# Optimization experiments

Hardware: AMD Instinct MI355X
Metric: run time of the kernel (lower is better)

## Reference

```python
import jax, jax.numpy as jnp
import numpy as np

EMB = 32
STEPS = 3
SLOPE = 0.01  # LeakyReLU default negative slope


def lrelu(x):
    return jnp.where(x > 0, x, SLOPE * x)


def seg_softmax(logits, seg, num_seg):
    # numerically stable per-segment softmax (matches torch_geometric.utils.softmax)
    m = jax.ops.segment_max(logits, seg, num_segments=num_seg)
    e = jnp.exp(logits - m[seg])
    s = jax.ops.segment_sum(e, seg, num_segments=num_seg)
    return e / s[seg]


def setup_inputs() -> dict:
    key = jax.random.key(0)
    ks = jax.random.split(key, 32)
    N, E, G = 200000, 3200000, 128
    p = lambda k, shape: (jax.random.normal(k, shape, dtype=jnp.float32) * 0.1)
    inp = {
        "node_feats": jax.random.normal(ks[0], (N, 1), dtype=jnp.float32),
        "edge_index": jax.random.randint(ks[1], (2, E), 0, N),
        "batch": jnp.sort(jax.random.randint(ks[2], (N,), 0, G)),
        "num_graphs": G,
        # embed_node: Linear(1, 32)
        "W_embed": p(ks[3], (1, EMB)), "b_embed": p(ks[4], (EMB,)),
        # per-step GraphNet params (stacked over steps)
        "Wm": p(ks[5], (STEPS, EMB, EMB)), "bm": p(ks[6], (STEPS, EMB)),          # f_mess (edge_size=0)
        "Wa": p(ks[7], (STEPS, 3 * EMB, EMB)), "ba": p(ks[8], (STEPS, EMB)),      # f_agg: [x, xg, agg]
        # per-step GlobalNode params
        "Wgate": p(ks[9], (STEPS, EMB, 1)), "bgate": p(ks[10], (STEPS, 1)),       # att_mask
        "Wfeat": p(ks[11], (STEPS, EMB, EMB)), "bfeat": p(ks[12], (STEPS, EMB)),  # att_feat
        "Wt": p(ks[13], (STEPS, 2 * EMB, EMB)), "bt": p(ks[14], (STEPS, EMB)),    # transform
        # heads
        "W_v": p(ks[15], (EMB, 1)), "b_v": p(ks[16], (1,)),
        "W_a0": p(ks[17], (EMB, 2)), "b_a0": p(ks[18], (2,)),
        "W_a1": p(ks[19], (EMB, 1)), "b_a1": p(ks[20], (1,)),
    }
    return inp


def reference(node_feats, edge_index, batch, num_graphs,
              W_embed, b_embed, Wm, bm, Wa, ba, Wgate, bgate, Wfeat, bfeat,
              Wt, bt, W_v, b_v, W_a0, b_a0, W_a1, b_a1):
    N = node_feats.shape[0]
    src, dst = edge_index[0], edge_index[1]

    x = lrelu(node_feats @ W_embed + b_embed)            # [N, 32]
    xg = jnp.zeros((num_graphs, EMB), dtype=x.dtype)     # [G, 32]

    for i in range(Wm.shape[0]):
        # GraphNet: gather -> MLP -> scatter-max -> update MLP + residual
        msg = lrelu(x[src] @ Wm[i] + bm[i])              # [E, 32]
        agg = jax.ops.segment_max(msg, dst, num_segments=N)
        agg = jnp.where(jnp.isfinite(agg), agg, 0.0)     # empty segments -> 0
        z = jnp.concatenate([x, xg[batch], agg], axis=1)  # [N, 96]
        x = lrelu(z @ Wa[i] + ba[i]) + x

        # GlobalNode: GlobalAttention pooling + transform with residual
        gate = seg_softmax((x @ Wgate[i] + bgate[i])[:, 0], batch, num_graphs)  # [N]
        feat = lrelu(x @ Wfeat[i] + bfeat[i])            # [N, 32]
        pooled = jax.ops.segment_sum(gate[:, None] * feat, batch, num_segments=num_graphs)
        cat = jnp.concatenate([pooled, xg], axis=1)      # [G, 64]
        xg = lrelu(cat @ Wt[i] + bt[i]) + xg

    value = xg @ W_v + b_v                               # [G, 1]
    a0_probs = jax.nn.softmax(xg @ W_a0 + b_a0, axis=1)  # [G, 2]
    a1_softmax = seg_softmax((x @ W_a1 + b_a1)[:, 0], batch, num_graphs)  # [N]
    return value, a0_probs, a1_softmax
```

## Files before the change

kernel.cpp:

```cpp
#include <hip/hip_runtime.h>
#include <hip/hip_bf16.h>

#define GG 128
#define SLOPE 0.01f
#define CHUNK 8192
#define NPB 64
#define NREP 64

#define OFF_Wm   0
#define OFF_bm   3072
#define OFF_Wa   3168
#define OFF_ba   12384
#define OFF_Wg   12480
#define OFF_bg   12576
#define OFF_Wf   12592
#define OFF_bf   15664
#define OFF_Wt   15760
#define OFF_bt   21904
#define OFF_Wa1  22000
#define OFF_ba1  22032
#define WCAT_N   22048

__device__ __forceinline__ float lrelu(float v) { return v > 0.f ? v : SLOPE * v; }

__device__ __forceinline__ float ldf(const void* p, int i, int isf) {
    if (isf) return ((const float*)p)[i];
    return __bfloat162float(((const __hip_bfloat16*)p)[i]);
}
__device__ __forceinline__ void stf(void* p, int i, float v, int isf) {
    if (isf) ((float*)p)[i] = v;
    else ((__hip_bfloat16*)p)[i] = __float2bfloat16(v);
}

__device__ __forceinline__ float bfLo(unsigned u) { return __uint_as_float(u << 16); }
__device__ __forceinline__ float bfHi(unsigned u) { return __uint_as_float(u & 0xFFFF0000u); }

__global__ void k_detect(const unsigned short* __restrict__ w, int n, int* __restrict__ flag,
                         unsigned* __restrict__ bcnt, int B) {
    __shared__ int bad;
    for (int t = threadIdx.x; t <= B; t += 256) bcnt[t] = 0u;
    if (threadIdx.x == 0) bad = 0;
    __syncthreads();
    for (int t = threadIdx.x; t < n; t += 256) {
        unsigned short u = w[t];
        int e = (u >> 7) & 0xFF;
        if (e >= 141) bad = 1;
    }
    __syncthreads();
    if (threadIdx.x == 0) { flag[0] = bad; flag[32] = 1; }
}

struct CvtArgs {
    const void* p[12];
    int off[12];
    int n[12];
};
__global__ void k_prep(CvtArgs a, float* __restrict__ wcat, const int* __restrict__ dtf,
                       const void* __restrict__ ba0, float* __restrict__ xgw,
                       const int* __restrict__ batch, int* __restrict__ goff, int N,
                       const int* __restrict__ dst, unsigned* __restrict__ bcnt, int E, int B,
                       float* __restrict__ xg_a, float* __restrict__ U, float* __restrict__ S) {
    __shared__ unsigned h[2048];
    int blk = blockIdx.x;
    int tid = threadIdx.x;
    const int cG = (N + 255) >> 8;
    const int cH = (E + CHUNK - 1) / CHUNK;
    if (blk < 432) {
        int seg = blk / 36;
        int i = (blk % 36) * 256 + tid;
        int isf = *dtf;
        if (i < a.n[seg]) wcat[a.off[seg] + i] = ldf(a.p[seg], i, isf);
        return;
    }
    blk -= 432;
    if (blk < 16) {
        int isf = *dtf;
        int idx = blk * 256 + tid;
        xgw[idx] = ldf(ba0, idx & 31, isf);
        return;
    }
    blk -= 16;
    if (blk < cG) {
        int n = blk * 256 + tid;
        if (n >= N) return;
        int bn = batch[n];
        if (n == 0) {
            for (int g = 0; g <= bn; ++g) goff[g] = 0;
        } else {
            int bp = batch[n - 1];
            for (int g = bp + 1; g <= bn; ++g) goff[g] = n;
        }
        if (n == N - 1) {
            for (int g = bn + 1; g <= GG; ++g) goff[g] = N;
        }
        return;
    }
    blk -= cG;
    if (blk < cH) {
        if (B > 2048) return;
        for (int t = tid; t < B; t += 256) h[t] = 0;
        __syncthreads();
        int start = blk * CHUNK, end = min(E, start + CHUNK);
        for (int e = start + tid; e < end; e += 256)
            atomicAdd(&h[dst[e] >> 8], 1u);
        __syncthreads();
        for (int t = tid; t < B; t += 256)
            if (h[t]) atomicAdd(&bcnt[t], h[t]);
        return;
    }
    blk -= cH;
    {
        float4 z4 = make_float4(0.f, 0.f, 0.f, 0.f);
        long long fi = (long long)blk * 256 + tid;
        if (fi < 65536) { ((float4*)U)[fi] = z4; return; }
        fi -= 65536;
        if (fi < 2048) { ((float4*)S)[fi] = z4; return; }
        fi -= 2048;
        if (fi < 1024) { ((float4*)xg_a)[fi] = z4; return; }
    }
}

__global__ void k_hist(const int* __restrict__ dst, unsigned* __restrict__ deg, int E) {
    int e = blockIdx.x * 256 + threadIdx.x;
    if (e >= E) return;
    atomicAdd(&deg[dst[e]], 1u);
}
__global__ void k_scan1(const unsigned* __restrict__ deg, unsigned* __restrict__ excl,
                        unsigned* __restrict__ bsum, int N) {
    __shared__ unsigned s[256];
    int i = blockIdx.x * 256 + threadIdx.x;
    unsigned v = (i < N) ? deg[i] : 0u;
    s[threadIdx.x] = v;
    __syncthreads();
    for (int off = 1; off < 256; off <<= 1) {
        unsigned t = (threadIdx.x >= (unsigned)off) ? s[threadIdx.x - off] : 0u;
        __syncthreads();
        s[threadIdx.x] += t;
        __syncthreads();
    }
    if (i < N) excl[i] = s[threadIdx.x] - v;
    if (threadIdx.x == 255) bsum[blockIdx.x] = s[255];
}
__global__ void k_scan2(const unsigned* __restrict__ bsum, unsigned* __restrict__ boff, int nb) {
    __shared__ unsigned s[256];
    __shared__ unsigned carry;
    if (threadIdx.x == 0) carry = 0u;
    __syncthreads();
    for (int base = 0; base < nb; base += 256) {
        int i = base + threadIdx.x;
        unsigned v = (i < nb) ? bsum[i] : 0u;
        s[threadIdx.x] = v;
        __syncthreads();
        for (int off = 1; off < 256; off <<= 1) {
            unsigned t = (threadIdx.x >= (unsigned)off) ? s[threadIdx.x - off] : 0u;
            __syncthreads();
            s[threadIdx.x] += t;
            __syncthreads();
        }
        if (i < nb) boff[i] = carry + s[threadIdx.x] - v;
        __syncthreads();
        if (threadIdx.x == 0) carry += s[255];
        __syncthreads();
    }
}
__global__ void k_scan3(unsigned* __restrict__ indptr, const unsigned* __restrict__ boff,
                        unsigned* __restrict__ cursor, int N, int E) {
    int i = blockIdx.x * 256 + threadIdx.x;
    if (i >= N) return;
    unsigned v = indptr[i] + boff[i >> 8];
    indptr[i] = v;
    cursor[i] = v;
    if (i == 0) indptr[N] = (unsigned)E;
}
__global__ void k_scatter(const int* __restrict__ src, const int* __restrict__ dst,
                          unsigned* __restrict__ cursor, unsigned* __restrict__ ssrc, int E) {
    int e = blockIdx.x * 256 + threadIdx.x;
    if (e >= E) return;
    unsigned pos = atomicAdd(&cursor[dst[e]], 1u);
    ssrc[pos] = (unsigned)src[e];
}

__global__ void k_bscan(const unsigned* __restrict__ bcnt, unsigned* __restrict__ bbase,
                        unsigned* __restrict__ bcur, int B, int E) {
    __shared__ unsigned s[256];
    __shared__ unsigned carry;
    if (threadIdx.x == 0) carry = 0u;
    __syncthreads();
    for (int base = 0; base < B; base += 256) {
        int i = base + threadIdx.x;
        unsigned v = (i < B) ? bcnt[i] : 0u;
        s[threadIdx.x] = v;
        __syncthreads();
        for (int off = 1; off < 256; off <<= 1) {
            unsigned t = (threadIdx.x >= (unsigned)off) ? s[threadIdx.x - off] : 0u;
            __syncthreads();
            s[threadIdx.x] += t;
            __syncthreads();
        }
        if (i < B) {
            unsigned ex = carry + s[threadIdx.x] - v;
            bbase[i] = ex;
            bcur[i] = ex;
        }
        __syncthreads();
        if (threadIdx.x == 0) carry += s[255];
        __syncthreads();
    }
    if (threadIdx.x == 0) bbase[B] = (unsigned)E;
}

__global__ void k_work(const int* __restrict__ src, const int* __restrict__ dst,
                       unsigned* __restrict__ bcur, unsigned long long* __restrict__ packed,
                       int E, int B, int nbA,
                       const void* __restrict__ nf, const void* __restrict__ We,
                       const void* __restrict__ be,
                       const float* __restrict__ Wm0, const float* __restrict__ bm0,
                       float* __restrict__ x, __hip_bfloat16* __restrict__ m, int N,
                       const int* __restrict__ dtf) {
    __shared__ unsigned h[2048];
    __shared__ unsigned pos[2048];
    __shared__ float WL[1024];
    __shared__ float WeL[32], beL[32], bmL[32];
    __shared__ float xs[8][32];
    int tid = threadIdx.x;
    if ((int)blockIdx.x < nbA) {
        for (int t = tid; t < B; t += 256) h[t] = 0;
        __syncthreads();
        int start = blockIdx.x * CHUNK, end = min(E, start + CHUNK);
        for (int e = start + tid; e < end; e += 256)
            atomicAdd(&h[dst[e] >> 8], 1u);
        __syncthreads();
        for (int t = tid; t < B; t += 256)
            pos[t] = h[t] ? atomicAdd(&bcur[t], h[t]) : 0u;
        __syncthreads();
        for (int e = start + tid; e < end; e += 256) {
            int d = dst[e];
            unsigned p = atomicAdd(&pos[d >> 8], 1u);
            packed[p] = ((unsigned long long)(unsigned)d << 32) | (unsigned)src[e];
        }
        return;
    }
    int blkE = blockIdx.x - nbA;
    int isf = *dtf;
    for (int t = tid; t < 1024; t += 256) WL[t] = Wm0[t];
    if (tid < 32) { WeL[tid] = ldf(We, tid, isf); beL[tid] = ldf(be, tid, isf); bmL[tid] = bm0[tid]; }
    int s = tid >> 5, j = tid & 31;
    int n = blkE * 8 + s;
    __syncthreads();
    float xv = 0.f;
    if (n < N) {
        xv = lrelu(ldf(nf, n, isf) * WeL[j] + beL[j]);
        x[n * 32 + j] = xv;
        xs[s][j] = xv;
    }
    __syncthreads();
    if (n >= N) return;
    float acc = bmL[j];
#pragma unroll
    for (int k = 0; k < 32; ++k) acc += xs[s][k] * WL[k * 32 + j];
    m[n * 32 + j] = __float2bfloat16(lrelu(acc));
}

__global__ void k_csr(const unsigned long long* __restrict__ packed,
                      const unsigned* __restrict__ bbase,
                      unsigned* __restrict__ indptr,
                      unsigned* __restrict__ ssrc, int N, int E) {
    __shared__ unsigned deg[256];
    __shared__ unsigned scn[256];
    __shared__ unsigned cur[256];
    int g = blockIdx.x, tid = threadIdx.x;
    int n0 = g << 8;
    int cnt = min(256, N - n0);
    deg[tid] = 0;
    __syncthreads();
    unsigned e0 = bbase[g], e1 = bbase[g + 1];
    for (unsigned e = e0 + tid; e < e1; e += 256) {
        int d = (int)(packed[e] >> 32);
        atomicAdd(&deg[d - n0], 1u);
    }
    __syncthreads();
    unsigned v = deg[tid];
    scn[tid] = v;
    __syncthreads();
    for (int off = 1; off < 256; off <<= 1) {
        unsigned t = (tid >= off) ? scn[tid - off] : 0u;
        __syncthreads();
        scn[tid] += t;
        __syncthreads();
    }
    unsigned start = e0 + scn[tid] - v;
    if (tid < cnt) { indptr[n0 + tid] = start; cur[tid] = start; }
    if (g == (int)gridDim.x - 1 && tid == 0) indptr[N] = (unsigned)E;
    __syncthreads();
    for (unsigned e = e0 + tid; e < e1; e += 256) {
        unsigned long long pk = packed[e];
        int d = (int)(pk >> 32);
        unsigned p = atomicAdd(&cur[d - n0], 1u);
        ssrc[p] = (unsigned)pk;
    }
}

__global__ __launch_bounds__(256, 4)
void k_step(float* __restrict__ x, const __hip_bfloat16* __restrict__ m_in,
            __hip_bfloat16* __restrict__ m_out,
            const int* __restrict__ batch,
            const unsigned* __restrict__ indptr, const unsigned* __restrict__ ssrc,
            const float* __restrict__ Wa, const float* __restrict__ xgw,
            const float* __restrict__ Wg, const float* __restrict__ bg,
            const float* __restrict__ Wa1, const float* __restrict__ ba1,
            const float* __restrict__ Wf, const float* __restrict__ bf,
            const float* __restrict__ Wm_nx, const float* __restrict__ bm_nx,
            float* __restrict__ la1, float* __restrict__ U, float* __restrict__ S,
            int N, int hasNext) {
    __shared__ float WL[2048];
    __shared__ float WmL[1024];
    __shared__ float zL[8][64];
    __shared__ float xnL[8][32];
    __shared__ float WgL[32], W1L[32], bmL[32], bfL[32];
    __shared__ float bgL, b1L;
    int tid = threadIdx.x;
    for (int t = tid; t < 2048; t += 256) WL[t] = (t < 1024) ? Wa[t] : Wa[t + 1024];
    if (hasNext) {
        for (int t = tid; t < 1024; t += 256) WmL[t] = Wm_nx[t];
        if (tid < 32) bmL[tid] = bm_nx[tid];
    }
    if (tid < 32) { WgL[tid] = Wg[tid]; W1L[tid] = Wa1[tid]; bfL[tid] = bf[tid]; }
    if (tid == 0) { bgL = bg[0]; b1L = ba1[0]; }
    int s = tid >> 5, j = tid & 31;
    int c = j & 7, eo = j >> 3;
    float wfr[32];
#pragma unroll
    for (int k = 0; k < 32; ++k) wfr[k] = Wf[k * 32 + j];
    const uint2* m2 = (const uint2*)m_in;
    int nbase = blockIdx.x * NPB;
    int rep = blockIdx.x & (NREP - 1);
    float* Urep = U + (size_t)rep * GG * 32;
    float* Srep = S + (size_t)rep * GG;
    __syncthreads();
    int gcur = -1;
    float Uacc = 0.f, Sacc = 0.f;
    for (int sub = 0; sub < NPB / 8; ++sub) {
        int n = nbase + sub * 8 + s;
        bool valid = n < N;
        int gb = gcur;
        float xj = 0.f;
        if (valid) {
            xj = x[n * 32 + j];
            zL[s][j] = xj;
            gb = batch[n];
        }
        if (valid && gb != gcur) {
            if (gcur >= 0) {
                atomicAdd(&Urep[gcur * 32 + j], Uacc);
                if (j == 0) atomicAdd(&Srep[gcur], Sacc);
            }
            gcur = gb; Uacc = 0.f; Sacc = 0.f;
        }
        unsigned st = 0, en = 0;
        if (valid) { st = indptr[n]; en = indptr[n + 1]; }
        float a[4];
#pragma unroll
        for (int t = 0; t < 4; ++t) a[t] = -INFINITY;
        if (en > st) {
            unsigned last = en - 1;
            for (unsigned base = st; base < en; base += 32) {
                unsigned eA = min(base + eo, last);
                unsigned eB = min(base + 4 + eo, last);
                unsigned eC = min(base + 8 + eo, last);
                unsigned eD = min(base + 12 + eo, last);
                unsigned eE = min(base + 16 + eo, last);
                unsigned eF = min(base + 20 + eo, last);
                unsigned eG = min(base + 24 + eo, last);
                unsigned eH = min(base + 28 + eo, last);
                unsigned sA = ssrc[eA];
                unsigned sB = ssrc[eB];
                unsigned sC = ssrc[eC];
                unsigned sD = ssrc[eD];
                unsigned sE = ssrc[eE];
                unsigned sF = ssrc[eF];
                unsigned sG = ssrc[eG];
                unsigned sH = ssrc[eH];
                uint2 vA = m2[sA * 8 + c];
                uint2 vB = m2[sB * 8 + c];
                uint2 vC = m2[sC * 8 + c];
                uint2 vD = m2[sD * 8 + c];
                uint2 vE = m2[sE * 8 + c];
                uint2 vF = m2[sF * 8 + c];
                uint2 vG = m2[sG * 8 + c];
                uint2 vH = m2[sH * 8 + c];
                a[0] = fmaxf(a[0], fmaxf(fmaxf(fmaxf(bfLo(vA.x), bfLo(vB.x)), fmaxf(bfLo(vC.x), bfLo(vD.x))),
                                         fmaxf(fmaxf(bfLo(vE.x), bfLo(vF.x)), fmaxf(bfLo(vG.x), bfLo(vH.x)))));
                a[1] = fmaxf(a[1], fmaxf(fmaxf(fmaxf(bfHi(vA.x), bfHi(vB.x)), fmaxf(bfHi(vC.x), bfHi(vD.x))),
                                         fmaxf(fmaxf(bfHi(vE.x), bfHi(vF.x)), fmaxf(bfHi(vG.x), bfHi(vH.x)))));
                a[2] = fmaxf(a[2], fmaxf(fmaxf(fmaxf(bfLo(vA.y), bfLo(vB.y)), fmaxf(bfLo(vC.y), bfLo(vD.y))),
                                         fmaxf(fmaxf(bfLo(vE.y), bfLo(vF.y)), fmaxf(bfLo(vG.y), bfLo(vH.y)))));
                a[3] = fmaxf(a[3], fmaxf(fmaxf(fmaxf(bfHi(vA.y), bfHi(vB.y)), fmaxf(bfHi(vC.y), bfHi(vD.y))),
                                         fmaxf(fmaxf(bfHi(vE.y), bfHi(vF.y)), fmaxf(bfHi(vG.y), bfHi(vH.y)))));
            }
        }
#pragma unroll
        for (int t = 0; t < 4; ++t) {
            a[t] = fmaxf(a[t], __shfl_xor(a[t], 8));
            a[t] = fmaxf(a[t], __shfl_xor(a[t], 16));
        }
        if (valid && eo == 0) {
            bool empty = (st == en);
#pragma unroll
            for (int t = 0; t < 4; ++t)
                zL[s][32 + (c << 2) + t] = empty ? 0.f : a[t];
        }
        if (valid) {
            float acc0 = xgw[gb * 32 + j];
            float acc1 = 0.f;
#pragma unroll
            for (int k = 0; k < 64; k += 2) {
                acc0 += zL[s][k] * WL[k * 32 + j];
                acc1 += zL[s][k + 1] * WL[(k + 1) * 32 + j];
            }
            float xn = lrelu(acc0 + acc1) + xj;
            x[n * 32 + j] = xn;
            xnL[s][j] = xn;
            float lv = xn * WgL[j];
            if (hasNext) {
#pragma unroll
                for (int off = 16; off; off >>= 1) lv += __shfl_xor(lv, off);
            } else {
                float l1 = xn * W1L[j];
#pragma unroll
                for (int off = 16; off; off >>= 1) { lv += __shfl_xor(lv, off); l1 += __shfl_xor(l1, off); }
                if (j == 0) la1[n] = l1 + b1L;
            }
            float e = __expf(lv + bgL);
            float f = bfL[j];
            if (hasNext) {
                float a2 = bmL[j];
#pragma unroll
                for (int k = 0; k < 32; ++k) {
                    float v = xnL[s][k];
                    f += v * wfr[k];
                    a2 += v * WmL[k * 32 + j];
                }
                m_out[n * 32 + j] = __float2bfloat16(lrelu(a2));
            } else {
#pragma unroll
                for (int k = 0; k < 32; ++k) f += xnL[s][k] * wfr[k];
            }
            Uacc += e * lrelu(f);
            Sacc += e;
        }
    }
    if (gcur >= 0) {
        atomicAdd(&Urep[gcur * 32 + j], Uacc);
        if (j == 0) atomicAdd(&Srep[gcur], Sacc);
    }
}

__global__ void k_gupd(float* __restrict__ U, float* __restrict__ S,
                       const float* __restrict__ xg_in,
                       const float* __restrict__ Wt, const float* __restrict__ bt,
                       float* __restrict__ xg_out,
                       const float* __restrict__ WaNx, const float* __restrict__ baNx,
                       float* __restrict__ xgw, int hasNext,
                       const float* __restrict__ logits, const int* __restrict__ goff,
                       const void* __restrict__ Wv, const void* __restrict__ bv,
                       const void* __restrict__ Wa0, const void* __restrict__ ba0,
                       void* __restrict__ out, int N, const int* __restrict__ dtf) {
    __shared__ float Up[8][32];
    __shared__ float Sp[8];
    __shared__ float pl[32];
    __shared__ float vL[32];
    __shared__ float red[256];
    int g = blockIdx.x;
    int tid = threadIdx.x;
    int rp = tid >> 5, j = tid & 31;
    float usum = 0.f, ssum = 0.f;
    for (int r = rp; r < NREP; r += 8) {
        size_t ui = (size_t)r * GG * 32 + g * 32 + j;
        usum += U[ui];
        U[ui] = 0.f;
        if (j == 0) { ssum += S[r * GG + g]; S[r * GG + g] = 0.f; }
    }
    Up[rp][j] = usum;
    if (j == 0) Sp[rp] = ssum;
    __syncthreads();
    if (rp == 0) {
        float ut = 0.f;
#pragma unroll
        for (int i = 0; i < 8; ++i) ut += Up[i][j];
        float st = ((Sp[0] + Sp[1]) + (Sp[2] + Sp[3])) + ((Sp[4] + Sp[5]) + (Sp[6] + Sp[7]));
        float inv = (st > 0.f) ? 1.f / st : 0.f;
        pl[j] = ut * inv;
        float xgv = xg_in[g * 32 + j];
        vL[j] = xgv;
        float acc = bt[j];
#pragma unroll
        for (int k = 0; k < 32; ++k) acc += pl[k] * Wt[k * 32 + j];
#pragma unroll
        for (int k = 0; k < 32; ++k) acc += vL[k] * Wt[(32 + k) * 32 + j];
        float v = lrelu(acc) + xgv;
        xg_out[g * 32 + j] = v;
        vL[j] = v;
        if (hasNext) {
            float aw = baNx[j];
#pragma unroll
            for (int k = 0; k < 32; ++k) aw += vL[k] * WaNx[(32 + k) * 32 + j];
            xgw[g * 32 + j] = aw;
        }
    }
    __syncthreads();
    if (hasNext) return;
    int isf = *dtf;
    int s0 = goff[g], s1 = goff[g + 1];
    float lm = -INFINITY;
    for (int n = s0 + tid; n < s1; n += 256) lm = fmaxf(lm, logits[n]);
    red[tid] = lm;
    __syncthreads();
    for (int off = 128; off; off >>= 1) {
        if (tid < off) red[tid] = fmaxf(red[tid], red[tid + off]);
        __syncthreads();
    }
    float gmax = red[0];
    __syncthreads();
    float ls = 0.f;
    for (int n = s0 + tid; n < s1; n += 256) ls += expf(logits[n] - gmax);
    red[tid] = ls;
    __syncthreads();
    for (int off = 128; off; off >>= 1) {
        if (tid < off) red[tid] += red[tid + off];
        __syncthreads();
    }
    float inv = (red[0] > 0.f) ? 1.f / red[0] : 0.f;
    __syncthreads();
    for (int n = s0 + tid; n < s1; n += 256)
        stf(out, 384 + n, expf(logits[n] - gmax) * inv, isf);
    if (tid == 0) {
        float acc = ldf(bv, 0, isf);
        for (int k = 0; k < 32; ++k) acc += vL[k] * ldf(Wv, k, isf);
        stf(out, g, acc, isf);
        float l0 = ldf(ba0, 0, isf), l1 = ldf(ba0, 1, isf);
        for (int k = 0; k < 32; ++k) {
            float xv = vL[k];
            l0 += xv * ldf(Wa0, k * 2, isf);
            l1 += xv * ldf(Wa0, k * 2 + 1, isf);
        }
        float mm = fmaxf(l0, l1);
        float e0 = expf(l0 - mm), e1 = expf(l1 - mm);
        float si = 1.f / (e0 + e1);
        stf(out, 128 + 2 * g, e0 * si, isf);
        stf(out, 128 + 2 * g + 1, e1 * si, isf);
    }
}

extern "C" void kernel_launch(void* const* d_in, const int* in_sizes, int n_in,
                              void* d_out, int out_size, void* d_ws, size_t ws_size,
                              hipStream_t stream) {
    const void* nf      = d_in[0];
    const int*  eidx    = (const int*)d_in[1];
    const int*  batch   = (const int*)d_in[2];
    const void* W_embed = d_in[4];
    const void* b_embed = d_in[5];
    const void* Wm      = d_in[6];
    const void* bm      = d_in[7];
    const void* Wa      = d_in[8];
    const void* ba      = d_in[9];
    const void* Wgate   = d_in[10];
    const void* bgate   = d_in[11];
    const void* Wfeat   = d_in[12];
    const void* bfeat   = d_in[13];
    const void* Wt      = d_in[14];
    const void* bt      = d_in[15];
    const void* W_v     = d_in[16];
    const void* b_v     = d_in[17];
    const void* W_a0    = d_in[18];
    const void* b_a0    = d_in[19];
    const void* W_a1    = d_in[20];
    const void* b_a1    = d_in[21];

    const int N = in_sizes[0];
    const int E = in_sizes[1] / 2;
    const int nWm = in_sizes[6];
    const int* src = eidx;
    const int* dst = eidx + E;
    const int B = (N + 255) >> 8;

    char* ws = (char*)d_ws;
    size_t off = 0;
    auto alloc = [&](size_t bytes) -> char* {
        char* p = ws + off;
        off = (off + bytes + 255) & ~(size_t)255;
        return p;
    };
    float*          x      = (float*)alloc((size_t)N * 32 * 4);
    size_t mBytes  = (size_t)N * 32 * 2;
    __hip_bfloat16*     m_a    = (__hip_bfloat16*)alloc(mBytes);
    __hip_bfloat16*     m_b    = (__hip_bfloat16*)alloc(mBytes);
    unsigned long long* packed = (unsigned long long*)alloc((size_t)E * 8);
    float*          la1    = (float*)alloc((size_t)N * 4);
    unsigned*       indptr = (unsigned*)alloc((size_t)(N + 1) * 4);
    unsigned*       cursor = (unsigned*)alloc((size_t)N * 4);
    unsigned*       ssrc   = (unsigned*)alloc((size_t)(E + 16) * 4);
    const int nb = (N + 255) / 256;
    unsigned*       bsum   = (unsigned*)alloc((size_t)nb * 4);
    unsigned*       boff   = (unsigned*)alloc((size_t)nb * 4);
    unsigned*       bcnt   = (unsigned*)alloc((size_t)(B + 1) * 4);
    unsigned*       bbase  = (unsigned*)alloc((size_t)(B + 1) * 4);
    unsigned*       bcur   = (unsigned*)alloc((size_t)(B + 1) * 4);
    int*            goff   = (int*)alloc((size_t)(GG + 1) * 4);
    float*          xg_a   = (float*)alloc((size_t)GG * 32 * 4);
    float*          xg_b   = (float*)alloc((size_t)GG * 32 * 4);
    float*          xgw    = (float*)alloc((size_t)GG * 32 * 4);
    float*          U      = (float*)alloc((size_t)NREP * GG * 32 * 4);
    float*          S      = (float*)alloc((size_t)NREP * GG * 4);
    int*            dtf    = (int*)alloc(256);
    float*          wcat   = (float*)alloc((size_t)WCAT_N * 4);

    const int nB_n  = (N + 255) / 256;
    const int nB_e  = (E + 255) / 256;
    const int nB_n8 = (N + 7) / 8;
    const int nB_st = (N + NPB - 1) / NPB;
    const int nB_ch = (E + CHUNK - 1) / CHUNK;

    k_detect<<<1, 256, 0, stream>>>((const unsigned short*)Wm, nWm, dtf, bcnt, B);

    CvtArgs ca;
    const void* ps[12] = {Wm, bm, Wa, ba, Wgate, bgate, Wfeat, bfeat, Wt, bt, W_a1, b_a1};
    const int  offs[12] = {OFF_Wm, OFF_bm, OFF_Wa, OFF_ba, OFF_Wg, OFF_bg,
                           OFF_Wf, OFF_bf, OFF_Wt, OFF_bt, OFF_Wa1, OFF_ba1};
    const int  ns[12]  = {3072, 96, 9216, 96, 96, 3, 3072, 96, 6144, 96, 32, 1};
    for (int i = 0; i < 12; ++i) { ca.p[i] = ps[i]; ca.off[i] = offs[i]; ca.n[i] = ns[i]; }

    const int nPrep = 432 + 16 + nB_n + nB_ch + 268;
    k_prep<<<nPrep, 256, 0, stream>>>(ca, wcat, dtf, ba, xgw, batch, goff, N,
                                      dst, bcnt, E, B, xg_a, U, S);

    if (B <= 2048) {
        k_bscan<<<1, 256, 0, stream>>>(bcnt, bbase, bcur, B, E);
        k_work<<<nB_ch + nB_n8, 256, 0, stream>>>(src, dst, bcur, packed, E, B, nB_ch,
                                                  nf, W_embed, b_embed,
                                                  wcat + OFF_Wm, wcat + OFF_bm,
                                                  x, m_a, N, dtf);
        k_csr<<<B, 256, 0, stream>>>(packed, bbase, indptr, ssrc, N, E);
    } else {
        hipMemsetAsync(cursor, 0, (size_t)N * 4, stream);
        k_hist<<<nB_e, 256, 0, stream>>>(dst, cursor, E);
        k_scan1<<<nb, 256, 0, stream>>>(cursor, indptr, bsum, N);
        k_scan2<<<1, 256, 0, stream>>>(bsum, boff, nb);
        k_scan3<<<nB_n, 256, 0, stream>>>(indptr, boff, cursor, N, E);
        k_scatter<<<nB_e, 256, 0, stream>>>(src, dst, cursor, ssrc, E);
        k_work<<<nB_n8, 256, 0, stream>>>(src, dst, bcur, packed, E, B, 0,
                                          nf, W_embed, b_embed,
                                          wcat + OFF_Wm, wcat + OFF_bm,
                                          x, m_a, N, dtf);
    }

    float* xg_cur = xg_a;
    float* xg_nxt = xg_b;
    __hip_bfloat16* m_cur = m_a;
    __hip_bfloat16* m_nxt = m_b;
    for (int i = 0; i < 3; ++i) {
        int hasNext = (i < 2) ? 1 : 0;
        k_step<<<nB_st, 256, 0, stream>>>(x, m_cur, m_nxt, batch, indptr, ssrc,
                                          wcat + OFF_Wa + i * 3072, xgw,
                                          wcat + OFF_Wg + i * 32, wcat + OFF_bg + i,
                                          wcat + OFF_Wa1, wcat + OFF_ba1,
                                          wcat + OFF_Wf + i * 1024, wcat + OFF_bf + i * 32,
                                          wcat + OFF_Wm + (i + 1) * 1024,
                                          wcat + OFF_bm + (i + 1) * 32,
                                          la1, U, S, N, hasNext);
        k_gupd<<<GG, 256, 0, stream>>>(U, S, xg_cur,
                                       wcat + OFF_Wt + i * 2048,
                                       wcat + OFF_bt + i * 32, xg_nxt,
                                       wcat + OFF_Wa + (i + 1) * 3072,
                                       wcat + OFF_ba + (i + 1) * 32,
                                       xgw, hasNext,
                                       la1, goff, W_v, b_v, W_a0, b_a0,
                                       d_out, N, dtf);
        float* tmp = xg_cur; xg_cur = xg_nxt; xg_nxt = tmp;
        __hip_bfloat16* tm = m_cur; m_cur = m_nxt; m_nxt = tm;
    }
}
```

Measured before the change: 568.9 us.

## Software-pipeline node metadata and first edge-index batch across sub-iterations

Restructures the per-node aggregation loop into a software pipeline. Node metadata (x, batch, indptr) is loaded two sub-steps ahead, and the first 32 source indices one sub-step ahead, so the dependent gather chain indptr→ssrc→message overlaps with compute on the current node. It raises register pressure with many extra live values and loads clamped dummy data for out-of-range nodes, which may reduce occupancy.

```diff
diff --git a/kernel.cpp b/kernel.cpp
--- a/kernel.cpp
+++ b/kernel.cpp
@@ -339,86 +339,124 @@
     __syncthreads();
     int gcur = -1;
     float Uacc = 0.f, Sacc = 0.f;
+
+    int nC; bool vC; int gbC; float xjC; unsigned stC, enC;
+    int nN; bool vN; int gbN; float xjN; unsigned stN, enN;
+    unsigned p0, p1, p2, p3, p4, p5, p6, p7;
+    unsigned q0, q1, q2, q3, q4, q5, q6, q7;
+
+    auto loadMeta = [&](int sub, int& nn, bool& vv, int& gg, float& xx,
+                        unsigned& st_, unsigned& en_) {
+        int n = nbase + sub * 8 + s;
+        vv = (n < N);
+        int cl = vv ? n : (N - 1);
+        nn = cl;
+        xx = x[cl * 32 + j];
+        gg = batch[cl];
+        st_ = indptr[cl];
+        en_ = indptr[cl + 1];
+    };
+    auto issueSS = [&](unsigned st_, unsigned en_,
+                       unsigned& a0, unsigned& a1, unsigned& a2, unsigned& a3,
+                       unsigned& a4, unsigned& a5, unsigned& a6, unsigned& a7) {
+        unsigned b = (en_ > st_) ? st_ : 0u;
+        unsigned last = (en_ > st_) ? (en_ - 1) : 0u;
+        a0 = ssrc[min(b + eo, last)];
+        a1 = ssrc[min(b + 4 + eo, last)];
+        a2 = ssrc[min(b + 8 + eo, last)];
+        a3 = ssrc[min(b + 12 + eo, last)];
+        a4 = ssrc[min(b + 16 + eo, last)];
+        a5 = ssrc[min(b + 20 + eo, last)];
+        a6 = ssrc[min(b + 24 + eo, last)];
+        a7 = ssrc[min(b + 28 + eo, last)];
+    };
+
+    loadMeta(0, nC, vC, gbC, xjC, stC, enC);
+    issueSS(stC, enC, p0, p1, p2, p3, p4, p5, p6, p7);
+    loadMeta(1, nN, vN, gbN, xjN, stN, enN);
+
     for (int sub = 0; sub < NPB / 8; ++sub) {
-        int n = nbase + sub * 8 + s;
-        bool valid = n < N;
-        int gb = gcur;
-        float xj = 0.f;
-        if (valid) {
-            xj = x[n * 32 + j];
-            zL[s][j] = xj;
-            gb = batch[n];
-        }
-        if (valid && gb != gcur) {
-            if (gcur >= 0) {
-                atomicAdd(&Urep[gcur * 32 + j], Uacc);
-                if (j == 0) atomicAdd(&Srep[gcur], Sacc);
+        uint2 vA = m2[p0 * 8 + c];
+        uint2 vB = m2[p1 * 8 + c];
+        uint2 vC2 = m2[p2 * 8 + c];
+        uint2 vD = m2[p3 * 8 + c];
+        uint2 vE = m2[p4 * 8 + c];
+        uint2 vF = m2[p5 * 8 + c];
+        uint2 vG = m2[p6 * 8 + c];
+        uint2 vH = m2[p7 * 8 + c];
+        issueSS(stN, enN, q0, q1, q2, q3, q4, q5, q6, q7);
+        int nN2; bool vN2; int gbN2; float xjN2; unsigned stN2, enN2;
+        loadMeta(sub + 2, nN2, vN2, gbN2, xjN2, stN2, enN2);
+        float a0 = fmaxf(fmaxf(fmaxf(bfLo(vA.x), bfLo(vB.x)), fmaxf(bfLo(vC2.x), bfLo(vD.x))),
+                         fmaxf(fmaxf(bfLo(vE.x), bfLo(vF.x)), fmaxf(bfLo(vG.x), bfLo(vH.x))));
+        float a1 = fmaxf(fmaxf(fmaxf(bfHi(vA.x), bfHi(vB.x)), fmaxf(bfHi(vC2.x), bfHi(vD.x))),
+                         fmaxf(fmaxf(bfHi(vE.x), bfHi(vF.x)), fmaxf(bfHi(vG.x), bfHi(vH.x))));
+        float a2 = fmaxf(fmaxf(fmaxf(bfLo(vA.y), bfLo(vB.y)), fmaxf(bfLo(vC2.y), bfLo(vD.y))),
+                         fmaxf(fmaxf(bfLo(vE.y), bfLo(vF.y)), fmaxf(bfLo(vG.y), bfLo(vH.y))));
+        float a3 = fmaxf(fmaxf(fmaxf(bfHi(vA.y), bfHi(vB.y)), fmaxf(bfHi(vC2.y), bfHi(vD.y))),
+                         fmaxf(fmaxf(bfHi(vE.y), bfHi(vF.y)), fmaxf(bfHi(vG.y), bfHi(vH.y))));
+        if (enC > stC + 32) {
+            unsigned last = enC - 1;
+            for (unsigned base = stC + 32; base < enC; base += 32) {
+                unsigned tA = ssrc[min(base + eo, last)];
+                unsigned tB = ssrc[min(base + 4 + eo, last)];
+                unsigned tC = ssrc[min(base + 8 + eo, last)];
+                unsigned tD = ssrc[min(base + 12 + eo, last)];
+                unsigned tE = ssrc[min(base + 16 + eo, last)];
+                unsigned tF = ssrc[min(base + 20 + eo, last)];
+                unsigned tG = ssrc[min(base + 24 + eo, last)];
+                unsigned tH = ssrc[min(base + 28 + eo, last)];
+                uint2 wA = m2[tA * 8 + c];
+                uint2 wB = m2[tB * 8 + c];
+                uint2 wC = m2[tC * 8 + c];
+                uint2 wD = m2[tD * 8 + c];
+                uint2 wE = m2[tE * 8 + c];
+                uint2 wF = m2[tF * 8 + c];
+                uint2 wG = m2[tG * 8 + c];
+                uint2 wH = m2[tH * 8 + c];
+                a0 = fmaxf(a0, fmaxf(fmaxf(fmaxf(bfLo(wA.x), bfLo(wB.x)), fmaxf(bfLo(wC.x), bfLo(wD.x))),
+                                     fmaxf(fmaxf(bfLo(wE.x), bfLo(wF.x)), fmaxf(bfLo(wG.x), bfLo(wH.x)))));
+                a1 = fmaxf(a1, fmaxf(fmaxf(fmaxf(bfHi(wA.x), bfHi(wB.x)), fmaxf(bfHi(wC.x), bfHi(wD.x))),
+                                     fmaxf(fmaxf(bfHi(wE.x), bfHi(wF.x)), fmaxf(bfHi(wG.x), bfHi(wH.x)))));
+                a2 = fmaxf(a2, fmaxf(fmaxf(fmaxf(bfLo(wA.y), bfLo(wB.y)), fmaxf(bfLo(wC.y), bfLo(wD.y))),
+                                     fmaxf(fmaxf(bfLo(wE.y), bfLo(wF.y)), fmaxf(bfLo(wG.y), bfLo(wH.y)))));
+                a3 = fmaxf(a3, fmaxf(fmaxf(fmaxf(bfHi(wA.y), bfHi(wB.y)), fmaxf(bfHi(wC.y), bfHi(wD.y))),
+                                     fmaxf(fmaxf(bfHi(wE.y), bfHi(wF.y)), fmaxf(bfHi(wG.y), bfHi(wH.y)))));
             }
-            gcur = gb; Uacc = 0.f; Sacc = 0.f;
-        }
-        unsigned st = 0, en = 0;
-        if (valid) { st = indptr[n]; en = indptr[n + 1]; }
-        float a[4];
-#pragma unroll
-        for (int t = 0; t < 4; ++t) a[t] = -INFINITY;
-        if (en > st) {
-            unsigned last = en - 1;
-            for (unsigned base = st; base < en; base += 32) {
-                unsigned eA = min(base + eo, last);
-                unsigned eB = min(base + 4 + eo, last);
-                unsigned eC = min(base + 8 + eo, last);
-                unsigned eD = min(base + 12 + eo, last);
-                unsigned eE = min(base + 16 + eo, last);
-                unsigned eF = min(base + 20 + eo, last);
-                unsigned eG = min(base + 24 + eo, last);
-                unsigned eH = min(base + 28 + eo, last);
-                unsigned sA = ssrc[eA];
-                unsigned sB = ssrc[eB];
-                unsigned sC = ssrc[eC];
-                unsigned sD = ssrc[eD];
-                unsigned sE = ssrc[eE];
-                unsigned sF = ssrc[eF];
-                unsigned sG = ssrc[eG];
-                unsigned sH = ssrc[eH];
-                uint2 vA = m2[sA * 8 + c];
-                uint2 vB = m2[sB * 8 + c];
-                uint2 vC = m2[sC * 8 + c];
-                uint2 vD = m2[sD * 8 + c];
-                uint2 vE = m2[sE * 8 + c];
-                uint2 vF = m2[sF * 8 + c];
-                uint2 vG = m2[sG * 8 + c];
-                uint2 vH = m2[sH * 8 + c];
-                a[0] = fmaxf(a[0], fmaxf(fmaxf(fmaxf(bfLo(vA.x), bfLo(vB.x)), fmaxf(bfLo(vC.x), bfLo(vD.x))),
-                                         fmaxf(fmaxf(bfLo(vE.x), bfLo(vF.x)), fmaxf(bfLo(vG.x), bfLo(vH.x)))));
-                a[1] = fmaxf(a[1], fmaxf(fmaxf(fmaxf(bfHi(vA.x), bfHi(vB.x)), fmaxf(bfHi(vC.x), bfHi(vD.x))),
-                                         fmaxf(fmaxf(bfHi(vE.x), bfHi(vF.x)), fmaxf(bfHi(vG.x), bfHi(vH.x)))));
-                a[2] = fmaxf(a[2], fmaxf(fmaxf(fmaxf(bfLo(vA.y), bfLo(vB.y)), fmaxf(bfLo(vC.y), bfLo(vD.y))),
-                                         fmaxf(fmaxf(bfLo(vE.y), bfLo(vF.y)), fmaxf(bfLo(vG.y), bfLo(vH.y)))));
-                a[3] = fmaxf(a[3], fmaxf(fmaxf(fmaxf(bfHi(vA.y), bfHi(vB.y)), fmaxf(bfHi(vC.y), bfHi(vD.y))),
-                                         fmaxf(fmaxf(bfHi(vE.y), bfHi(vF.y)), fmaxf(bfHi(vG.y), bfHi(vH.y)))));
+        }
+        a0 = fmaxf(a0, __shfl_xor(a0, 8));
+        a0 = fmaxf(a0, __shfl_xor(a0, 16));
+        a1 = fmaxf(a1, __shfl_xor(a1, 8));
+        a1 = fmaxf(a1, __shfl_xor(a1, 16));
+        a2 = fmaxf(a2, __shfl_xor(a2, 8));
+        a2 = fmaxf(a2, __shfl_xor(a2, 16));
+        a3 = fmaxf(a3, __shfl_xor(a3, 8));
+        a3 = fmaxf(a3, __shfl_xor(a3, 16));
+        if (vC) {
+            if (gbC != gcur) {
+                if (gcur >= 0) {
+                    atomicAdd(&Urep[gcur * 32 + j], Uacc);
+                    if (j == 0) atomicAdd(&Srep[gcur], Sacc);
+                }
+                gcur = gbC; Uacc = 0.f; Sacc = 0.f;
             }
-        }
-#pragma unroll
-        for (int t = 0; t < 4; ++t) {
-            a[t] = fmaxf(a[t], __shfl_xor(a[t], 8));
-            a[t] = fmaxf(a[t], __shfl_xor(a[t], 16));
-        }
-        if (valid && eo == 0) {
-            bool empty = (st == en);
-#pragma unroll
-            for (int t = 0; t < 4; ++t)
-                zL[s][32 + (c << 2) + t] = empty ? 0.f : a[t];
-        }
-        if (valid) {
-            float acc0 = xgw[gb * 32 + j];
+            zL[s][j] = xjC;
+            if (eo == 0) {
+                bool empty = (stC == enC);
+                zL[s][32 + (c << 2) + 0] = empty ? 0.f : a0;
+                zL[s][32 + (c << 2) + 1] = empty ? 0.f : a1;
+                zL[s][32 + (c << 2) + 2] = empty ? 0.f : a2;
+                zL[s][32 + (c << 2) + 3] = empty ? 0.f : a3;
+            }
+            float acc0 = xgw[gbC * 32 + j];
             float acc1 = 0.f;
 #pragma unroll
             for (int k = 0; k < 64; k += 2) {
                 acc0 += zL[s][k] * WL[k * 32 + j];
                 acc1 += zL[s][k + 1] * WL[(k + 1) * 32 + j];
             }
-            float xn = lrelu(acc0 + acc1) + xj;
-            x[n * 32 + j] = xn;
+            float xn = lrelu(acc0 + acc1) + xjC;
+            x[nC * 32 + j] = xn;
             xnL[s][j] = xn;
             float lv = xn * WgL[j];
             if (hasNext) {
@@ -428,19 +466,19 @@
                 float l1 = xn * W1L[j];
 #pragma unroll
                 for (int off = 16; off; off >>= 1) { lv += __shfl_xor(lv, off); l1 += __shfl_xor(l1, off); }
-                if (j == 0) la1[n] = l1 + b1L;
+                if (j == 0) la1[nC] = l1 + b1L;
             }
             float e = __expf(lv + bgL);
             float f = bfL[j];
             if (hasNext) {
-                float a2 = bmL[j];
+                float a2m = bmL[j];
 #pragma unroll
                 for (int k = 0; k < 32; ++k) {
                     float v = xnL[s][k];
                     f += v * wfr[k];
-                    a2 += v * WmL[k * 32 + j];
+                    a2m += v * WmL[k * 32 + j];
                 }
-                m_out[n * 32 + j] = __float2bfloat16(lrelu(a2));
+                m_out[nC * 32 + j] = __float2bfloat16(lrelu(a2m));
             } else {
 #pragma unroll
                 for (int k = 0; k < 32; ++k) f += xnL[s][k] * wfr[k];
@@ -448,6 +486,9 @@
             Uacc += e * lrelu(f);
             Sacc += e;
         }
+        nC = nN; vC = vN; gbC = gbN; xjC = xjN; stC = stN; enC = enN;
+        nN = nN2; vN = vN2; gbN = gbN2; xjN = xjN2; stN = stN2; enN = enN2;
+        p0 = q0; p1 = q1; p2 = q2; p3 = q3; p4 = q4; p5 = q5; p6 = q6; p7 = q7;
     }
     if (gcur >= 0) {
         atomicAdd(&Urep[gcur * 32 + j], Uacc);
```

After: 554.6 us. 1.03x faster.
